# Performance work log

Measured on AMD Instinct MI355X. Metric: run time of the kernel, lower is better.

## Reference

```python
import jax, jax.numpy as jnp
import numpy as np

B, C, H, W = 2, 256, 64, 64
HEADS = 8
HEAD_DIM = C // HEADS  # 32
INNER = HEADS * HEAD_DIM  # 256
GROUPS = 32
EPS = 1e-5


def groupnorm(x, w, b):
    # x: [B, C, H, W]; normalize over (C//G, H, W) within each of G groups
    Bx, Cx, Hx, Wx = x.shape
    xg = x.reshape(Bx, GROUPS, -1)
    mu = xg.mean(axis=-1, keepdims=True)
    var = xg.var(axis=-1, keepdims=True)
    xn = ((xg - mu) * jax.lax.rsqrt(var + EPS)).reshape(Bx, Cx, Hx, Wx)
    return xn * w[:, None, None] + b[:, None, None]


def setup_inputs() -> dict:
    key = jax.random.key(0)
    k0, k1, k2 = jax.random.split(key, 3)
    x = jax.random.normal(k0, (B, C, H, W), dtype=jnp.float32)
    gn_weight = jnp.ones((C,), dtype=jnp.float32)
    gn_bias = jnp.zeros((C,), dtype=jnp.float32)
    # 1x1 conv weights (kernel dims squeezed): [out_ch, in_ch]
    w_qkv = jax.random.normal(k1, (3 * INNER, C), dtype=jnp.float32) * 0.02
    w_out = jax.random.normal(k2, (C, INNER), dtype=jnp.float32) * 0.02
    return {"x": x, "gn_weight": gn_weight, "gn_bias": gn_bias,
            "w_qkv": w_qkv, "w_out": w_out}


def reference(x, gn_weight, gn_bias, w_qkv, w_out):
    Bx, Cx, Hx, Wx = x.shape
    N = Hx * Wx
    scale = HEAD_DIM ** -0.5
    xn = groupnorm(x, gn_weight, gn_bias)
    # 1x1 conv == channel matmul
    qkv = jnp.einsum('oc,bchw->bohw', w_qkv, xn)  # [B, 3*INNER, H, W]
    q, k, v = jnp.split(qkv, 3, axis=1)
    # 'b (h d) x y -> b h (x y) d'
    def to_heads(t):
        return t.reshape(Bx, HEADS, HEAD_DIM, N).transpose(0, 1, 3, 2)  # bhnd
    q, k, v = to_heads(q), to_heads(k), to_heads(v)
    sim = jnp.einsum('bhid,bhjd->bhij', q, k) * scale  # [B, h, N, N]
    attn = jax.nn.softmax(sim, axis=-1)
    o = jnp.einsum('bhij,bhjd->bhid', attn, v)  # [B, h, N, d]
    # 'b h (x y) d -> b (h d) x y'
    o = o.transpose(0, 1, 3, 2).reshape(Bx, INNER, Hx, Wx)
    out = jnp.einsum('co,bohw->bchw', w_out, o)
    return x + out
```

## Files before the change

kernel.cpp:

```cpp
#include <hip/hip_runtime.h>
#include <hip/hip_bf16.h>

#define BATCH 2
#define CH 256
#define HW 4096
#define HEADS 8
#define HDIM 32
#define GROUPS 32
#define EPS 1e-5f
#define SCALE 0.17677669529663687f
#define QSCALE (0.17677669529663687f * 1.4426950408889634f)

typedef short s16x8 __attribute__((ext_vector_type(8)));
typedef float floatx4 __attribute__((ext_vector_type(4)));
typedef unsigned short ushort_t;
typedef unsigned int uint_t;

static __device__ __forceinline__ ushort_t f2bf(float f) {
    __hip_bfloat16 h = __float2bfloat16(f);
    return *reinterpret_cast<ushort_t*>(&h);
}

static __device__ __forceinline__ uint_t pk2(float lo, float hi) {
    return __builtin_amdgcn_perm(__float_as_uint(hi), __float_as_uint(lo), 0x07060302u);
}

static __device__ __forceinline__ void gload_lds16(const ushort_t* g, ushort_t* l) {
    __builtin_amdgcn_global_load_lds((const __attribute__((address_space(1))) void*)g,
                                     (__attribute__((address_space(3))) void*)l, 16, 0, 0);
}

__global__ void gn_stats_wcvt(const float* __restrict__ x, float* __restrict__ stats,
                              const float* __restrict__ wq, const float* __restrict__ wo,
                              ushort_t* __restrict__ wdst) {
    if (blockIdx.x >= 64) {
        int i = (blockIdx.x - 64) * 256 + threadIdx.x;
        float4 v = (i < 49152) ? ((const float4*)wq)[i] : ((const float4*)wo)[i - 49152];
        ushort_t p[4] = {f2bf(v.x), f2bf(v.y), f2bf(v.z), f2bf(v.w)};
        uint2 o;
        o.x = (uint_t)p[0] | ((uint_t)p[1] << 16);
        o.y = (uint_t)p[2] | ((uint_t)p[3] << 16);
        *(uint2*)&wdst[(size_t)i * 4] = o;
        return;
    }
    int bg = blockIdx.x;
    const float4* xv = (const float4*)(x + (size_t)bg * 8 * HW);
    int t = threadIdx.x;
    float s = 0.f, ss = 0.f;
    for (int i = t; i < 8192; i += 256) {
        float4 v = xv[i];
        s  += v.x + v.y + v.z + v.w;
        ss += v.x*v.x + v.y*v.y + v.z*v.z + v.w*v.w;
    }
    #pragma unroll
    for (int off = 32; off; off >>= 1) {
        s  += __shfl_down(s, off);
        ss += __shfl_down(ss, off);
    }
    __shared__ float rs[4], rss[4];
    int wave = t >> 6;
    if ((t & 63) == 0) { rs[wave] = s; rss[wave] = ss; }
    __syncthreads();
    if (t == 0) {
        s  = rs[0] + rs[1] + rs[2] + rs[3];
        ss = rss[0] + rss[1] + rss[2] + rss[3];
        float mu  = s / 32768.f;
        float var = ss / 32768.f - mu * mu;
        stats[bg * 2]     = mu;
        stats[bg * 2 + 1] = rsqrtf(var + EPS);
    }
}

__global__ void norm_transpose(const float* __restrict__ x, const float* __restrict__ stats,
                               const float* __restrict__ gw, const float* __restrict__ gb,
                               ushort_t* __restrict__ xn) {
    __shared__ ushort_t tile[64][40];
    int b = blockIdx.z, c0 = blockIdx.y * 32, n0 = blockIdx.x * 64;
    int t = threadIdx.x;
    #pragma unroll
    for (int i = 0; i < 8; i++) {
        int idx = i * 256 + t;
        int c = idx >> 6, n = idx & 63;
        int cc = c0 + c;
        float mu   = stats[(b * GROUPS + (cc >> 3)) * 2];
        float rstd = stats[(b * GROUPS + (cc >> 3)) * 2 + 1];
        float v = x[((size_t)b * CH + cc) * HW + n0 + n];
        v = (v - mu) * rstd * gw[cc] + gb[cc];
        tile[n][c] = f2bf(v);
    }
    __syncthreads();
    int n = t >> 2, chk = t & 3;
    uint4 val = *(const uint4*)&tile[n][chk * 8];
    *(uint4*)(xn + ((size_t)(b * HW + n0 + n)) * CH + c0 + chk * 8) = val;
}

__global__ void qkv_gemm(const ushort_t* __restrict__ xn, const ushort_t* __restrict__ wqb,
                         ushort_t* __restrict__ qo, ushort_t* __restrict__ ko,
                         ushort_t* __restrict__ vo) {
    __shared__ ushort_t Al[64][40];
    __shared__ ushort_t Bl[64][40];
    int b = blockIdx.z;
    int n0 = blockIdx.x * 64, o0 = blockIdx.y * 64;
    int t = threadIdx.x, lane = t & 63, wave = t >> 6;
    int lr = lane & 15, lk = lane >> 4;
    int row = t >> 2, chk = t & 3;
    const ushort_t* asrc = xn + ((size_t)(b * HW + n0 + row)) * CH + chk * 8;
    const ushort_t* bsrc = wqb + (size_t)(o0 + row) * CH + chk * 8;
    floatx4 acc[4] = {};
    uint4 ra = *(const uint4*)(asrc);
    uint4 rb = *(const uint4*)(bsrc);
    for (int k0 = 0; k0 < 8; k0++) {
        *(uint4*)&Al[row][chk * 8] = ra;
        *(uint4*)&Bl[row][chk * 8] = rb;
        __syncthreads();
        if (k0 < 7) {
            ra = *(const uint4*)(asrc + (k0 + 1) * 32);
            rb = *(const uint4*)(bsrc + (k0 + 1) * 32);
        }
        s16x8 af = *(const s16x8*)&Al[wave * 16 + lr][lk * 8];
        #pragma unroll
        for (int ct = 0; ct < 4; ct++) {
            s16x8 bf = *(const s16x8*)&Bl[ct * 16 + lr][lk * 8];
            acc[ct] = __builtin_amdgcn_mfma_f32_16x16x32_bf16(af, bf, acc[ct], 0, 0, 0);
        }
        __syncthreads();
    }
    #pragma unroll
    for (int ct = 0; ct < 4; ct++) {
        int o = o0 + ct * 16 + lr;
        int sel = o >> 8;
        int h = (o >> 5) & 7;
        int d = o & 31;
        int nrow0 = n0 + wave * 16 + (lk << 2);
        if (sel == 0) {
            #pragma unroll
            for (int r = 0; r < 4; r++)
                qo[(((size_t)(b * HEADS + h)) * HW + nrow0 + r) * HDIM + d] =
                    f2bf(acc[ct][r] * QSCALE);
        } else if (sel == 1) {
            #pragma unroll
            for (int r = 0; r < 4; r++) {
                int tt = (nrow0 + r) & 63;
                int sg = 4 * ((tt >> 3) & 3) + 16 * ((((tt >> 2) & 1) << 1) | ((tt >> 5) & 1)) + (tt & 3);
                ko[(((size_t)(b * HEADS + h)) * HW + n0 + sg) * HDIM + d] = f2bf(acc[ct][r]);
            }
        } else {
            ushort_t pk[4];
            #pragma unroll
            for (int r = 0; r < 4; r++) pk[r] = f2bf(acc[ct][r]);
            *(uint2*)&vo[(((size_t)(b * HEADS + h)) * HDIM + d) * HW + nrow0] = *(uint2*)pk;
        }
    }
}

__global__ void __launch_bounds__(256, 4)
attn8(const ushort_t* __restrict__ qg, const ushort_t* __restrict__ kg,
      const ushort_t* __restrict__ vg, ushort_t* __restrict__ og) {
    __shared__ ushort_t Kl[2][2][2048];
    __shared__ ushort_t Vl[2][2][2048];
    const int bh = blockIdx.y;
    const int n0 = blockIdx.x * 64;
    const int t = threadIdx.x;
    const int lane = t & 63, w = t >> 6;
    const int lr = lane & 15, lk = lane >> 4;

    const ushort_t* kb = kg + (size_t)bh * HW * HDIM;
    const ushort_t* vb = vg + (size_t)bh * HDIM * HW;

    const int lrr = t & 15, lkk = (t >> 4) & 3, wv = t >> 6;
    const ushort_t* gkX = kb + ((wv << 4) + lrr) * HDIM + lkk * 8;
    const ushort_t* gkY = gkX + 64 * HDIM;
    const ushort_t* gvX = vb + (size_t)(((t >> 7) << 4) + lrr) * HW + ((t >> 6) & 1) * 32 + lkk * 8;
    const ushort_t* gvY = gvX + 64;
    ushort_t* kdX[2] = {&Kl[0][0][wv << 9], &Kl[1][0][wv << 9]};
    ushort_t* kdY[2] = {&Kl[0][1][wv << 9], &Kl[1][1][wv << 9]};
    ushort_t* vdX[2] = {&Vl[0][0][wv << 9], &Vl[1][0][wv << 9]};
    ushort_t* vdY[2] = {&Vl[0][1][wv << 9], &Vl[1][1][wv << 9]};

    s16x8 qf = *(const s16x8*)(qg + ((size_t)bh * HW + n0 + w * 16 + lr) * HDIM + lk * 8);

    const s16x8 onesf = {0x3F80, 0x3F80, 0x3F80, 0x3F80, 0x3F80, 0x3F80, 0x3F80, 0x3F80};
    const floatx4 zf = {};
    floatx4 oacc[2] = {};
    floatx4 Lacc = {};

    auto stage0 = [&]() {
        gload_lds16(gkX, kdX[0]); gload_lds16(gkY, kdY[0]);
        gload_lds16(gvX, vdX[0]); gload_lds16(gvY, vdY[0]);
        gkX += 128 * HDIM; gkY += 128 * HDIM; gvX += 128; gvY += 128;
    };
    auto stage1 = [&]() {
        gload_lds16(gkX, kdX[1]); gload_lds16(gkY, kdY[1]);
        gload_lds16(gvX, vdX[1]); gload_lds16(gvY, vdY[1]);
        gkX += 128 * HDIM; gkY += 128 * HDIM; gvX += 128; gvY += 128;
    };
    auto computeSub = [&](const ushort_t* Kb, const ushort_t* Vb) {
        floatx4 sim[4];
        __builtin_amdgcn_s_setprio(1);
#pragma unroll
        for (int ct = 0; ct < 4; ct++) {
            s16x8 kf = *(const s16x8*)(Kb + ct * 512 + lane * 8);
            sim[ct] = __builtin_amdgcn_mfma_f32_16x16x32_bf16(kf, qf, zf, 0, 0, 0);
        }
        __builtin_amdgcn_s_setprio(0);
        s16x8 vf[4];
#pragma unroll
        for (int i = 0; i < 4; i++)
            vf[i] = *(const s16x8*)(Vb + i * 512 + lane * 8);
        s16x8 pf[2];
#pragma unroll
        for (int s = 0; s < 2; s++) {
            union { uint_t u[4]; s16x8 v; } pu;
            pu.u[0] = pk2(__builtin_amdgcn_exp2f(sim[s][0]),     __builtin_amdgcn_exp2f(sim[s][1]));
            pu.u[1] = pk2(__builtin_amdgcn_exp2f(sim[s][2]),     __builtin_amdgcn_exp2f(sim[s][3]));
            pu.u[2] = pk2(__builtin_amdgcn_exp2f(sim[s + 2][0]), __builtin_amdgcn_exp2f(sim[s + 2][1]));
            pu.u[3] = pk2(__builtin_amdgcn_exp2f(sim[s + 2][2]), __builtin_amdgcn_exp2f(sim[s + 2][3]));
            pf[s] = pu.v;
        }
        __builtin_amdgcn_s_setprio(1);
#pragma unroll
        for (int s = 0; s < 2; s++) {
            oacc[0] = __builtin_amdgcn_mfma_f32_16x16x32_bf16(vf[s],     pf[s], oacc[0], 0, 0, 0);
            oacc[1] = __builtin_amdgcn_mfma_f32_16x16x32_bf16(vf[2 + s], pf[s], oacc[1], 0, 0, 0);
            Lacc    = __builtin_amdgcn_mfma_f32_16x16x32_bf16(onesf,     pf[s], Lacc,    0, 0, 0);
        }
        __builtin_amdgcn_s_setprio(0);
    };

#define SYNCF { asm volatile("s_waitcnt vmcnt(0)" ::: "memory"); __syncthreads(); }

    stage0();
    SYNCF
    for (int s2 = 0; s2 < 16; s2++) {
        stage1();
        computeSub(&Kl[0][0][0], &Vl[0][0][0]);
        computeSub(&Kl[0][1][0], &Vl[0][1][0]);
        SYNCF
        if (s2 < 15) {
            stage0();
            computeSub(&Kl[1][0][0], &Vl[1][0][0]);
            computeSub(&Kl[1][1][0], &Vl[1][1][0]);
            SYNCF
        } else {
            computeSub(&Kl[1][0][0], &Vl[1][0][0]);
            computeSub(&Kl[1][1][0], &Vl[1][1][0]);
        }
    }
#undef SYNCF

    const int b = bh >> 3, h = bh & 7;
    float inv = 1.0f / Lacc[0];
    int n = n0 + w * 16 + lr;
#pragma unroll
    for (int ct2 = 0; ct2 < 2; ct2++) {
        uint_t lo = (uint_t)f2bf(oacc[ct2][0] * inv) | ((uint_t)f2bf(oacc[ct2][1] * inv) << 16);
        uint_t hi = (uint_t)f2bf(oacc[ct2][2] * inv) | ((uint_t)f2bf(oacc[ct2][3] * inv) << 16);
        uint2 val = {lo, hi};
        *(uint2*)(og + ((size_t)b * HW + n) * CH + h * 32 + ct2 * 16 + lk * 4) = val;
    }
}

__global__ void proj_res(const ushort_t* __restrict__ oa, const ushort_t* __restrict__ wob,
                         const float* __restrict__ x, float* __restrict__ out) {
    __shared__ ushort_t Al[64][40];
    __shared__ ushort_t Bl[64][40];
    int m0 = blockIdx.x * 64;
    int c0 = blockIdx.y * 64;
    int t = threadIdx.x, lane = t & 63, wave = t >> 6;
    int lr = lane & 15, lk = lane >> 4;
    int row = t >> 2, chk = t & 3;
    const ushort_t* asrc = oa + (size_t)(m0 + row) * CH + chk * 8;
    const ushort_t* bsrc = wob + (size_t)(c0 + row) * CH + chk * 8;
    floatx4 acc[4] = {};
    uint4 ra = *(const uint4*)(asrc);
    uint4 rb = *(const uint4*)(bsrc);
    for (int k0 = 0; k0 < 8; k0++) {
        *(uint4*)&Al[row][chk * 8] = ra;
        *(uint4*)&Bl[row][chk * 8] = rb;
        __syncthreads();
        if (k0 < 7) {
            ra = *(const uint4*)(asrc + (k0 + 1) * 32);
            rb = *(const uint4*)(bsrc + (k0 + 1) * 32);
        }
        s16x8 af = *(const s16x8*)&Al[wave * 16 + lr][lk * 8];
        #pragma unroll
        for (int ct = 0; ct < 4; ct++) {
            s16x8 bf = *(const s16x8*)&Bl[ct * 16 + lr][lk * 8];
            acc[ct] = __builtin_amdgcn_mfma_f32_16x16x32_bf16(af, bf, acc[ct], 0, 0, 0);
        }
        __syncthreads();
    }
    int mrow0 = m0 + wave * 16 + (lk << 2);
    int b = mrow0 >> 12;
    int n = mrow0 & 4095;
    #pragma unroll
    for (int ct = 0; ct < 4; ct++) {
        int c = c0 + ct * 16 + lr;
        const float4 xv = *(const float4*)(x + ((size_t)(b * CH + c)) * HW + n);
        float4 ov;
        ov.x = acc[ct][0] + xv.x;
        ov.y = acc[ct][1] + xv.y;
        ov.z = acc[ct][2] + xv.z;
        ov.w = acc[ct][3] + xv.w;
        *(float4*)(out + ((size_t)(b * CH + c)) * HW + n) = ov;
    }
}

extern "C" void kernel_launch(void* const* d_in, const int* in_sizes, int n_in,
                              void* d_out, int out_size, void* d_ws, size_t ws_size,
                              hipStream_t stream) {
    const float* x    = (const float*)d_in[0];
    const float* gw   = (const float*)d_in[1];
    const float* gb   = (const float*)d_in[2];
    const float* wqkv = (const float*)d_in[3];
    const float* wout = (const float*)d_in[4];
    float* out = (float*)d_out;

    char* ws = (char*)d_ws;
    float* stats = (float*)ws;
    ushort_t* xn = (ushort_t*)(ws + 512);
    size_t per = (size_t)BATCH * HW * CH;
    ushort_t* q   = xn + per;
    ushort_t* k   = q + per;
    ushort_t* v   = k + per;
    ushort_t* oa  = v + per;
    ushort_t* wqb = oa + per;
    ushort_t* wob = wqb + 196608;

    gn_stats_wcvt<<<320, 256, 0, stream>>>(x, stats, wqkv, wout, wqb);
    norm_transpose<<<dim3(64, 8, 2), 256, 0, stream>>>(x, stats, gw, gb, xn);
    qkv_gemm<<<dim3(64, 12, 2), 256, 0, stream>>>(xn, wqb, q, k, v);
    attn8<<<dim3(64, 16), 256, 0, stream>>>(q, k, v, oa);
    proj_res<<<dim3(128, 4), 256, 0, stream>>>(oa, wob, x, out);
}
```

Baseline: 88.28 us.

## Process two query tiles per attention block to reuse K/V loads

Each attention workgroup now handles 128 queries (two 64-row Q fragments per wave) instead of 64, so every K/V tile staged in LDS feeds twice as many MFMAs. The K/V staging unit drops from 128 keys to 64 per stage, with twice as many loop iterations, and the grid is halved to 512 blocks. This roughly halves global K/V traffic and LDS fragment reads per unit of work, at the cost of more registers (launch bounds lowered to 2) and fewer blocks, which may leave some CUs underfilled.

```diff
diff --git a/kernel.cpp b/kernel.cpp
--- a/kernel.cpp
+++ b/kernel.cpp
@@ -153,13 +153,13 @@
     }
 }
 
-__global__ void __launch_bounds__(256, 4)
-attn8(const ushort_t* __restrict__ qg, const ushort_t* __restrict__ kg,
+__global__ void __launch_bounds__(256, 2)
+attn9(const ushort_t* __restrict__ qg, const ushort_t* __restrict__ kg,
       const ushort_t* __restrict__ vg, ushort_t* __restrict__ og) {
-    __shared__ ushort_t Kl[2][2][2048];
-    __shared__ ushort_t Vl[2][2][2048];
+    __shared__ ushort_t Kl[2][2048];
+    __shared__ ushort_t Vl[2][2048];
     const int bh = blockIdx.y;
-    const int n0 = blockIdx.x * 64;
+    const int n0 = blockIdx.x * 128;
     const int t = threadIdx.x;
     const int lane = t & 63, w = t >> 6;
     const int lr = lane & 15, lk = lane >> 4;
@@ -168,95 +168,111 @@
     const ushort_t* vb = vg + (size_t)bh * HDIM * HW;
 
     const int lrr = t & 15, lkk = (t >> 4) & 3, wv = t >> 6;
-    const ushort_t* gkX = kb + ((wv << 4) + lrr) * HDIM + lkk * 8;
-    const ushort_t* gkY = gkX + 64 * HDIM;
-    const ushort_t* gvX = vb + (size_t)(((t >> 7) << 4) + lrr) * HW + ((t >> 6) & 1) * 32 + lkk * 8;
-    const ushort_t* gvY = gvX + 64;
-    ushort_t* kdX[2] = {&Kl[0][0][wv << 9], &Kl[1][0][wv << 9]};
-    ushort_t* kdY[2] = {&Kl[0][1][wv << 9], &Kl[1][1][wv << 9]};
-    ushort_t* vdX[2] = {&Vl[0][0][wv << 9], &Vl[1][0][wv << 9]};
-    ushort_t* vdY[2] = {&Vl[0][1][wv << 9], &Vl[1][1][wv << 9]};
-
-    s16x8 qf = *(const s16x8*)(qg + ((size_t)bh * HW + n0 + w * 16 + lr) * HDIM + lk * 8);
+    const ushort_t* gk = kb + ((wv << 4) + lrr) * HDIM + lkk * 8;
+    const ushort_t* gv = vb + (size_t)(((t >> 7) << 4) + lrr) * HW + ((t >> 6) & 1) * 32 + lkk * 8;
+    ushort_t* kd0 = &Kl[0][wv << 9]; ushort_t* kd1 = &Kl[1][wv << 9];
+    ushort_t* vd0 = &Vl[0][wv << 9]; ushort_t* vd1 = &Vl[1][wv << 9];
+
+    s16x8 qf0 = *(const s16x8*)(qg + ((size_t)bh * HW + n0 + w * 16 + lr) * HDIM + lk * 8);
+    s16x8 qf1 = *(const s16x8*)(qg + ((size_t)bh * HW + n0 + 64 + w * 16 + lr) * HDIM + lk * 8);
+    asm volatile("s_waitcnt vmcnt(0)" ::: "memory");
 
     const s16x8 onesf = {0x3F80, 0x3F80, 0x3F80, 0x3F80, 0x3F80, 0x3F80, 0x3F80, 0x3F80};
     const floatx4 zf = {};
-    floatx4 oacc[2] = {};
-    floatx4 Lacc = {};
-
-    auto stage0 = [&]() {
-        gload_lds16(gkX, kdX[0]); gload_lds16(gkY, kdY[0]);
-        gload_lds16(gvX, vdX[0]); gload_lds16(gvY, vdY[0]);
-        gkX += 128 * HDIM; gkY += 128 * HDIM; gvX += 128; gvY += 128;
+    floatx4 oacc[2][2] = {};
+    floatx4 Lacc[2] = {};
+
+    auto stage = [&](ushort_t* kdn, ushort_t* vdn) {
+        gload_lds16(gk, kdn);
+        gload_lds16(gv, vdn);
+        gk += 64 * HDIM; gv += 64;
     };
-    auto stage1 = [&]() {
-        gload_lds16(gkX, kdX[1]); gload_lds16(gkY, kdY[1]);
-        gload_lds16(gvX, vdX[1]); gload_lds16(gvY, vdY[1]);
-        gkX += 128 * HDIM; gkY += 128 * HDIM; gvX += 128; gvY += 128;
-    };
-    auto computeSub = [&](const ushort_t* Kb, const ushort_t* Vb) {
-        floatx4 sim[4];
+    auto compute = [&](const ushort_t* Kb, const ushort_t* Vb) {
+        floatx4 sim0[4], sim1[4];
         __builtin_amdgcn_s_setprio(1);
 #pragma unroll
         for (int ct = 0; ct < 4; ct++) {
             s16x8 kf = *(const s16x8*)(Kb + ct * 512 + lane * 8);
-            sim[ct] = __builtin_amdgcn_mfma_f32_16x16x32_bf16(kf, qf, zf, 0, 0, 0);
+            sim0[ct] = __builtin_amdgcn_mfma_f32_16x16x32_bf16(kf, qf0, zf, 0, 0, 0);
+            sim1[ct] = __builtin_amdgcn_mfma_f32_16x16x32_bf16(kf, qf1, zf, 0, 0, 0);
         }
         __builtin_amdgcn_s_setprio(0);
         s16x8 vf[4];
 #pragma unroll
         for (int i = 0; i < 4; i++)
             vf[i] = *(const s16x8*)(Vb + i * 512 + lane * 8);
-        s16x8 pf[2];
-#pragma unroll
-        for (int s = 0; s < 2; s++) {
-            union { uint_t u[4]; s16x8 v; } pu;
-            pu.u[0] = pk2(__builtin_amdgcn_exp2f(sim[s][0]),     __builtin_amdgcn_exp2f(sim[s][1]));
-            pu.u[1] = pk2(__builtin_amdgcn_exp2f(sim[s][2]),     __builtin_amdgcn_exp2f(sim[s][3]));
-            pu.u[2] = pk2(__builtin_amdgcn_exp2f(sim[s + 2][0]), __builtin_amdgcn_exp2f(sim[s + 2][1]));
-            pu.u[3] = pk2(__builtin_amdgcn_exp2f(sim[s + 2][2]), __builtin_amdgcn_exp2f(sim[s + 2][3]));
-            pf[s] = pu.v;
-        }
-        __builtin_amdgcn_s_setprio(1);
-#pragma unroll
-        for (int s = 0; s < 2; s++) {
-            oacc[0] = __builtin_amdgcn_mfma_f32_16x16x32_bf16(vf[s],     pf[s], oacc[0], 0, 0, 0);
-            oacc[1] = __builtin_amdgcn_mfma_f32_16x16x32_bf16(vf[2 + s], pf[s], oacc[1], 0, 0, 0);
-            Lacc    = __builtin_amdgcn_mfma_f32_16x16x32_bf16(onesf,     pf[s], Lacc,    0, 0, 0);
-        }
-        __builtin_amdgcn_s_setprio(0);
+        {
+            s16x8 pf[2];
+#pragma unroll
+            for (int s = 0; s < 2; s++) {
+                union { uint_t u[4]; s16x8 v; } pu;
+                pu.u[0] = pk2(__builtin_amdgcn_exp2f(sim0[s][0]),     __builtin_amdgcn_exp2f(sim0[s][1]));
+                pu.u[1] = pk2(__builtin_amdgcn_exp2f(sim0[s][2]),     __builtin_amdgcn_exp2f(sim0[s][3]));
+                pu.u[2] = pk2(__builtin_amdgcn_exp2f(sim0[s + 2][0]), __builtin_amdgcn_exp2f(sim0[s + 2][1]));
+                pu.u[3] = pk2(__builtin_amdgcn_exp2f(sim0[s + 2][2]), __builtin_amdgcn_exp2f(sim0[s + 2][3]));
+                pf[s] = pu.v;
+            }
+            __builtin_amdgcn_s_setprio(1);
+#pragma unroll
+            for (int s = 0; s < 2; s++) {
+                oacc[0][0] = __builtin_amdgcn_mfma_f32_16x16x32_bf16(vf[s],     pf[s], oacc[0][0], 0, 0, 0);
+                oacc[0][1] = __builtin_amdgcn_mfma_f32_16x16x32_bf16(vf[2 + s], pf[s], oacc[0][1], 0, 0, 0);
+                Lacc[0]    = __builtin_amdgcn_mfma_f32_16x16x32_bf16(onesf,     pf[s], Lacc[0],    0, 0, 0);
+            }
+            __builtin_amdgcn_s_setprio(0);
+        }
+        {
+            s16x8 pf[2];
+#pragma unroll
+            for (int s = 0; s < 2; s++) {
+                union { uint_t u[4]; s16x8 v; } pu;
+                pu.u[0] = pk2(__builtin_amdgcn_exp2f(sim1[s][0]),     __builtin_amdgcn_exp2f(sim1[s][1]));
+                pu.u[1] = pk2(__builtin_amdgcn_exp2f(sim1[s][2]),     __builtin_amdgcn_exp2f(sim1[s][3]));
+                pu.u[2] = pk2(__builtin_amdgcn_exp2f(sim1[s + 2][0]), __builtin_amdgcn_exp2f(sim1[s + 2][1]));
+                pu.u[3] = pk2(__builtin_amdgcn_exp2f(sim1[s + 2][2]), __builtin_amdgcn_exp2f(sim1[s + 2][3]));
+                pf[s] = pu.v;
+            }
+            __builtin_amdgcn_s_setprio(1);
+#pragma unroll
+            for (int s = 0; s < 2; s++) {
+                oacc[1][0] = __builtin_amdgcn_mfma_f32_16x16x32_bf16(vf[s],     pf[s], oacc[1][0], 0, 0, 0);
+                oacc[1][1] = __builtin_amdgcn_mfma_f32_16x16x32_bf16(vf[2 + s], pf[s], oacc[1][1], 0, 0, 0);
+                Lacc[1]    = __builtin_amdgcn_mfma_f32_16x16x32_bf16(onesf,     pf[s], Lacc[1],    0, 0, 0);
+            }
+            __builtin_amdgcn_s_setprio(0);
+        }
     };
 
 #define SYNCF { asm volatile("s_waitcnt vmcnt(0)" ::: "memory"); __syncthreads(); }
 
-    stage0();
+    stage(kd0, vd0);
     SYNCF
-    for (int s2 = 0; s2 < 16; s2++) {
-        stage1();
-        computeSub(&Kl[0][0][0], &Vl[0][0][0]);
-        computeSub(&Kl[0][1][0], &Vl[0][1][0]);
+    for (int s2 = 0; s2 < 32; s2++) {
+        stage(kd1, vd1);
+        compute(&Kl[0][0], &Vl[0][0]);
         SYNCF
-        if (s2 < 15) {
-            stage0();
-            computeSub(&Kl[1][0][0], &Vl[1][0][0]);
-            computeSub(&Kl[1][1][0], &Vl[1][1][0]);
+        if (s2 < 31) {
+            stage(kd0, vd0);
+            compute(&Kl[1][0], &Vl[1][0]);
             SYNCF
         } else {
-            computeSub(&Kl[1][0][0], &Vl[1][0][0]);
-            computeSub(&Kl[1][1][0], &Vl[1][1][0]);
+            compute(&Kl[1][0], &Vl[1][0]);
         }
     }
 #undef SYNCF
 
     const int b = bh >> 3, h = bh & 7;
-    float inv = 1.0f / Lacc[0];
-    int n = n0 + w * 16 + lr;
-#pragma unroll
-    for (int ct2 = 0; ct2 < 2; ct2++) {
-        uint_t lo = (uint_t)f2bf(oacc[ct2][0] * inv) | ((uint_t)f2bf(oacc[ct2][1] * inv) << 16);
-        uint_t hi = (uint_t)f2bf(oacc[ct2][2] * inv) | ((uint_t)f2bf(oacc[ct2][3] * inv) << 16);
-        uint2 val = {lo, hi};
-        *(uint2*)(og + ((size_t)b * HW + n) * CH + h * 32 + ct2 * 16 + lk * 4) = val;
+#pragma unroll
+    for (int c = 0; c < 2; c++) {
+        float inv = 1.0f / Lacc[c][0];
+        int n = n0 + c * 64 + w * 16 + lr;
+#pragma unroll
+        for (int ct2 = 0; ct2 < 2; ct2++) {
+            uint_t lo = (uint_t)f2bf(oacc[c][ct2][0] * inv) | ((uint_t)f2bf(oacc[c][ct2][1] * inv) << 16);
+            uint_t hi = (uint_t)f2bf(oacc[c][ct2][2] * inv) | ((uint_t)f2bf(oacc[c][ct2][3] * inv) << 16);
+            uint2 val = {lo, hi};
+            *(uint2*)(og + ((size_t)b * HW + n) * CH + h * 32 + ct2 * 16 + lk * 4) = val;
+        }
     }
 }
 
@@ -330,6 +346,6 @@
     gn_stats_wcvt<<<320, 256, 0, stream>>>(x, stats, wqkv, wout, wqb);
     norm_transpose<<<dim3(64, 8, 2), 256, 0, stream>>>(x, stats, gw, gb, xn);
     qkv_gemm<<<dim3(64, 12, 2), 256, 0, stream>>>(xn, wqb, q, k, v);
-    attn8<<<dim3(64, 16), 256, 0, stream>>>(q, k, v, oa);
+    attn9<<<dim3(32, 16), 256, 0, stream>>>(q, k, v, oa);
     proj_res<<<dim3(128, 4), 256, 0, stream>>>(oa, wob, x, out);
 }
```

Result: no change. 88.88 us (+0.7%).
